# Optimization experiments

Measured on AMD Instinct MI355X. Metric: run time of the kernel, lower is better.

The kernel has to match this reference:

```python
import jax, jax.numpy as jnp
import numpy as np
import math

N = 131072   # number of points
C = 32       # embed_dim
K = 19       # num_class
ZD = 16      # z_dim
BN_EPS = 1e-4
SIG_THR = 0.8


def setup_inputs():
    key = jax.random.key(0)
    ks = jax.random.split(key, 16)
    f32 = jnp.float32
    rn = lambda k, s, sc=1.0: jax.random.normal(k, s, dtype=f32) * sc
    return {
        'feat': rn(ks[0], (N, C)),
        'scene_flow': rn(ks[1], (N, 3)),
        'coarse_pred': rn(ks[2], (N, K)),
        'z': rn(ks[3], (ZD,)),
        'select_w1': rn(ks[4], (C, C), 0.2),
        'bn_gamma': jnp.ones((C,), f32),
        'bn_beta': jnp.zeros((C,), f32),
        'bn_mean': jnp.zeros((C,), f32),
        'bn_var': jnp.ones((C,), f32),
        'select_w2': rn(ks[5], (C, 1), 0.2),
        'select_b2': jnp.zeros((1,), f32),
        'wq': rn(ks[6], (C, C), 0.2), 'bq': jnp.zeros((C,), f32),
        'wk': rn(ks[7], (C, C), 0.2), 'bk': jnp.zeros((C,), f32),
        'wv': rn(ks[8], (C, C), 0.2), 'bv': jnp.zeros((C,), f32),
        'wo': rn(ks[9], (C, C), 0.2), 'bo': jnp.zeros((C,), f32),
        'wt': rn(ks[10], (2 * C, C), 0.2), 'bt': jnp.zeros((C,), f32),
        'w_out': rn(ks[11], (C, K), 0.2), 'b_out': jnp.zeros((K,), f32),
        'w_gen': rn(ks[12], (ZD + K + 3, C), 0.2), 'b_gen': jnp.zeros((C,), f32),
    }


def _forward(feat, scene_flow, coarse_pred, z, select_w1, bn_gamma, bn_beta,
             bn_mean, bn_var, select_w2, select_b2, wq, bq, wk, bk, wv, bv,
             wo, bo, wt, bt, w_out, b_out, w_gen, b_gen):
    cp = jax.nn.softmax(coarse_pred, axis=-1)                      # (N, K)
    temp_mask = jnp.any(scene_flow != 0, axis=-1)                  # (N,)
    # select_mlp: Linear(no bias) -> BatchNorm(eval, eps=1e-4) -> ReLU -> Linear -> Sigmoid
    h = (feat @ select_w1 - bn_mean) / jnp.sqrt(bn_var + BN_EPS) * bn_gamma + bn_beta
    h = jnp.maximum(h, 0.0)
    score = jax.nn.sigmoid(h @ select_w2 + select_b2)[:, 0]        # (N,)
    valid = (score < SIG_THR) & temp_mask                          # (N,)
    # cvae stand-in: linear over concat(z, onehot(class), scene_flow) -> (N, K, C)
    wz, wc, ws = w_gen[:ZD], w_gen[ZD:ZD + K], w_gen[ZD + K:]
    gen = (z @ wz + b_gen)[None, None, :] + wc[None, :, :] + (scene_flow @ ws)[:, None, :]
    gen = gen * cp[:, :, None]                                     # scale by softmax prob
    # tiny cross-attention: 1 query per point over K=19 class prototypes
    q = feat @ wq + bq                                             # (N, C)
    k_ = jnp.einsum('nkc,cd->nkd', gen, wk) + bk                   # (N, K, C)
    v_ = jnp.einsum('nkc,cd->nkd', gen, wv) + bv                   # (N, K, C)
    attn = jax.nn.softmax(jnp.einsum('nd,nkd->nk', q, k_) / math.sqrt(C), axis=-1)
    aug = jnp.einsum('nk,nkd->nd', attn, v_) @ wo + bo             # (N, C)
    # scatter-back: invalid points get zeros (equivalent to torch boolean scatter)
    new_feat = jnp.where(valid[:, None], aug, 0.0)
    refine = jnp.concatenate([feat, new_feat], axis=-1) @ wt + bt  # (N, C)
    return refine @ w_out + b_out                                  # (N, K)


def reference(feat, scene_flow, coarse_pred, z, select_w1, bn_gamma, bn_beta,
              bn_mean, bn_var, select_w2, select_b2, wq, bq, wk, bk, wv, bv,
              wo, bo, wt, bt, w_out, b_out, w_gen, b_gen):
    return _forward(feat, scene_flow, coarse_pred, z, select_w1, bn_gamma,
                    bn_beta, bn_mean, bn_var, select_w2, select_b2, wq, bq,
                    wk, bk, wv, bv, wo, bo, wt, bt, w_out, b_out, w_gen, b_gen)
```

## Files before the change

kernel.cpp:

```cpp
#include <hip/hip_runtime.h>

#define NPTS 131072

constexpr int OFF_SW1 = 0;
constexpr int OFF_BNS = 1024;
constexpr int OFF_BNH = 1056;
constexpr int OFF_SW2 = 1088;
constexpr int OFF_B2  = 1120;
constexpr int TBL  = 1152;
constexpr int TQG  = 1152;
constexpr int TA1  = 1760;
constexpr int TGVB = 2368;
constexpr int TMVB = 2729;
constexpr int TQM  = 2786;
constexpr int TQBV = 2882;
constexpr int TQGB = 2914;
constexpr int TBB  = 2933;
constexpr int TCV  = 2952;
constexpr int TQMB = 2971;
constexpr int TQBB = 2974;
constexpr int LQG  = 0,    LA1  = 608,  LGVB = 1216, LMVB = 1577;
constexpr int LQM  = 1634, LQBV = 1730, LQGB = 1762, LBB  = 1781;
constexpr int LCV  = 1800, LQMB = 1819, LQBB = 1822;
constexpr int XG   = 3072;
constexpr int XA2  = 3680;
constexpr int XMK  = 4288;
constexpr int XMV  = 4384;
constexpr int XGK  = 4480;
constexpr int XGV  = 5088;
constexpr int XB   = 5696;

#define CONST_AS __attribute__((address_space(4)))
__device__ __forceinline__ const CONST_AS float* to_const(const float* p) {
    return (const CONST_AS float*)p;
}

__global__ __launch_bounds__(256) void pre_a(
    const float* __restrict__ z,
    const float* __restrict__ sw1,
    const float* __restrict__ bn_gamma, const float* __restrict__ bn_beta,
    const float* __restrict__ bn_mean,  const float* __restrict__ bn_var,
    const float* __restrict__ sw2,      const float* __restrict__ sb2,
    const float* __restrict__ wq, const float* __restrict__ bq,
    const float* __restrict__ wk, const float* __restrict__ bk,
    const float* __restrict__ wv,
    const float* __restrict__ wt, const float* __restrict__ bt,
    const float* __restrict__ wout, const float* __restrict__ bout,
    const float* __restrict__ wgen, const float* __restrict__ bgen,
    float* __restrict__ W)
{
    int i = blockIdx.x * 256 + threadIdx.x;
    if (i < 1024) {
        W[OFF_SW1 + i] = sw1[(i & 31) * 32 + (i >> 5)];
    } else if (i < 1632) {
        int t = i - 1024, e = t / 19, j = t % 19;
        float a1 = 0.f, a2 = 0.f;
        for (int d = 0; d < 32; ++d) {
            float w_ = wout[d*19 + j];
            a1 += wt[e*32 + d] * w_;
            a2 += wt[(32 + e)*32 + d] * w_;
        }
        W[TA1 + t] = a1; W[XA2 + t] = a2;
    } else if (i < 2240) {
        int t = i - 1632, k = t >> 5, e = t & 31;
        float g = bgen[e];
        for (int d = 0; d < 16; ++d) g += z[d] * wgen[d*32 + e];
        W[XG + t] = g + wgen[(16 + k)*32 + e];
    } else if (i < 2336) {
        int t = i - 2240, m = t >> 5, c = t & 31;
        float a = 0.f, b = 0.f;
        for (int e = 0; e < 32; ++e) {
            float wsr = wgen[(35 + m)*32 + e];
            a += wsr * wk[e*32 + c];
            b += wsr * wv[e*32 + c];
        }
        W[XMK + t] = a; W[XMV + t] = b;
    } else if (i < 2368) {
        int t = i - 2336;
        float scale = bn_gamma[t] / sqrtf(bn_var[t] + 1e-4f);
        W[OFF_BNS + t] = scale;
        W[OFF_BNH + t] = bn_beta[t] - bn_mean[t] * scale;
        W[OFF_SW2 + t] = sw2[t];
    } else if (i < 2387) {
        int t = i - 2368;
        float a = bout[t];
        for (int d = 0; d < 32; ++d) a += bt[d] * wout[d*19 + t];
        W[TBB + t] = a;
    } else if (i < 2419) {
        int t = i - 2387;
        float a = 0.f;
        for (int c = 0; c < 32; ++c) a += wq[t*32 + c] * bk[c];
        W[TQBV + t] = a;
    } else if (i == 2419) {
        W[OFF_B2] = sb2[0];
    } else if (i == 2420) {
        float a = 0.f;
        for (int c = 0; c < 32; ++c) a += bq[c] * bk[c];
        W[TQBB] = a;
    } else if (i == 2421) {
        W[TBL + 1823] = 0.f;
    }
}

__global__ __launch_bounds__(256) void pre_b(
    const float* __restrict__ wq, const float* __restrict__ bq,
    const float* __restrict__ wk, const float* __restrict__ wv,
    const float* __restrict__ wo,
    float* __restrict__ W)
{
    int i = blockIdx.x * 256 + threadIdx.x;
    if (i < 608) {
        int k = i >> 5, c = i & 31;
        float a = 0.f, b = 0.f;
        for (int e = 0; e < 32; ++e) {
            float g = W[XG + k*32 + e];
            a += g * wk[e*32 + c];
            b += g * wv[e*32 + c];
        }
        W[XGK + i] = a; W[XGV + i] = b;
    } else if (i < 1216) {
        int t = i - 608, c = t / 19, j = t % 19;
        float a = 0.f;
        for (int d = 0; d < 32; ++d) a += wo[c*32 + d] * W[XA2 + d*19 + j];
        W[XB + t] = a;
    } else if (i < 1312) {
        int t = i - 1216, e = t / 3, m = t % 3;
        float a = 0.f;
        for (int c = 0; c < 32; ++c) a += wq[e*32 + c] * W[XMK + m*32 + c];
        W[TQM + t] = a;
    } else if (i < 1315) {
        int m = i - 1312;
        float a = 0.f;
        for (int c = 0; c < 32; ++c) a += bq[c] * W[XMK + m*32 + c];
        W[TQMB + m] = a;
    }
}

__global__ __launch_bounds__(256) void pre_c(
    const float* __restrict__ wq, const float* __restrict__ bq,
    const float* __restrict__ bv, const float* __restrict__ bo,
    float* __restrict__ W)
{
    int i = blockIdx.x * 256 + threadIdx.x;
    if (i < 608) {
        int e = i / 19, k = i % 19;
        float a = 0.f;
        for (int c = 0; c < 32; ++c) a += wq[e*32 + c] * W[XGK + k*32 + c];
        W[TQG + i] = a;
    } else if (i < 627) {
        int k = i - 608;
        float a = 0.f;
        for (int c = 0; c < 32; ++c) a += bq[c] * W[XGK + k*32 + c];
        W[TQGB + k] = a;
    } else if (i < 988) {
        int t = i - 627, k = t / 19, j = t % 19;
        float a = 0.f;
        for (int c = 0; c < 32; ++c) a += W[XGV + k*32 + c] * W[XB + c*19 + j];
        W[TGVB + t] = a;
    } else if (i < 1045) {
        int t = i - 988, m = t / 19, j = t % 19;
        float a = 0.f;
        for (int c = 0; c < 32; ++c) a += W[XMV + m*32 + c] * W[XB + c*19 + j];
        W[TMVB + t] = a;
    } else if (i < 1064) {
        int j = i - 1045;
        float a = 0.f;
        for (int c = 0; c < 32; ++c) a += bv[c] * W[XB + c*19 + j];
        for (int d = 0; d < 32; ++d) a += bo[d] * W[XA2 + d*19 + j];
        W[TCV + j] = a;
    }
}

__global__ __launch_bounds__(256, 1) void main_k(
    const float* __restrict__ feat,
    const float* __restrict__ sflow,
    const float* __restrict__ cpred,
    const float* __restrict__ Wg,
    float* __restrict__ out)
{
    const CONST_AS float* W = to_const(Wg);
    const int n = blockIdx.x * 256 + threadIdx.x;
    const int t = threadIdx.x;

    __shared__ float T[1824];
    {
        const float4* src = (const float4*)(Wg + TBL);
        float4* dst = (float4*)T;
        dst[t] = src[t];
        if (t < 200) dst[256 + t] = src[256 + t];
    }
    __syncthreads();

    float f[32];
    const float4* fp = (const float4*)(feat + (long)n * 32);
#pragma unroll
    for (int g = 0; g < 8; ++g) {
        float4 v = fp[g];
        f[g*4+0] = v.x; f[g*4+1] = v.y; f[g*4+2] = v.z; f[g*4+3] = v.w;
    }
    float s0 = sflow[(long)n*3 + 0];
    float s1 = sflow[(long)n*3 + 1];
    float s2 = sflow[(long)n*3 + 2];
    bool tmask = (s0 != 0.f) | (s1 != 0.f) | (s2 != 0.f);

    float cp[19];
#pragma unroll
    for (int k = 0; k < 19; ++k) cp[k] = cpred[(long)n*19 + k];
    float m1 = cp[0];
#pragma unroll
    for (int k = 1; k < 19; ++k) m1 = fmaxf(m1, cp[k]);
    float sum1 = 0.f;
#pragma unroll
    for (int k = 0; k < 19; ++k) { cp[k] = __expf(cp[k] - m1); sum1 += cp[k]; }
    float r1 = 1.f / sum1;
#pragma unroll
    for (int k = 0; k < 19; ++k) cp[k] *= r1;

    float sacc = W[OFF_B2];
#pragma unroll
    for (int c = 0; c < 32; ++c) {
        float a = 0.f;
#pragma unroll
        for (int e = 0; e < 32; ++e) a = fmaf(f[e], W[OFF_SW1 + c*32 + e], a);
        float h = fmaf(a, W[OFF_BNS + c], W[OFF_BNH + c]);
        h = fmaxf(h, 0.f);
        sacc = fmaf(h, W[OFF_SW2 + c], sacc);
    }
    bool valid = tmask && (sacc < 1.3862943611198906f);

    float qg[19], o[19];
#pragma unroll
    for (int k = 0; k < 19; ++k) { qg[k] = T[LQGB + k]; o[k] = T[LBB + k]; }
    float qm0 = T[LQMB + 0], qm1 = T[LQMB + 1], qm2 = T[LQMB + 2];
    float qb = T[LQBB];
#pragma unroll 4
    for (int e = 0; e < 32; ++e) {
        float fe = f[e];
#pragma unroll
        for (int k = 0; k < 19; ++k) {
            qg[k] = fmaf(fe, T[LQG + e*19 + k], qg[k]);
            o[k]  = fmaf(fe, T[LA1 + e*19 + k], o[k]);
        }
        qm0 = fmaf(fe, T[LQM + e*3 + 0], qm0);
        qm1 = fmaf(fe, T[LQM + e*3 + 1], qm1);
        qm2 = fmaf(fe, T[LQM + e*3 + 2], qm2);
        qb  = fmaf(fe, T[LQBV + e], qb);
    }
    float qs = s0*qm0 + s1*qm1 + s2*qm2;

    const float RS = 0.17677669529663687f;
    float l[19];
#pragma unroll
    for (int k = 0; k < 19; ++k) l[k] = fmaf(cp[k], qg[k] + qs, qb) * RS;

    float m2 = l[0];
#pragma unroll
    for (int k = 1; k < 19; ++k) m2 = fmaxf(m2, l[k]);
    float sum2 = 0.f;
#pragma unroll
    for (int k = 0; k < 19; ++k) { l[k] = __expf(l[k] - m2); sum2 += l[k]; }
    float r2 = 1.f / sum2;
    float Sw = 0.f;
#pragma unroll
    for (int k = 0; k < 19; ++k) { l[k] = l[k] * r2 * cp[k]; Sw += l[k]; }

    float a2[19];
#pragma unroll
    for (int j = 0; j < 19; ++j) a2[j] = T[LCV + j];
    float cms[3] = { Sw * s0, Sw * s1, Sw * s2 };
#pragma unroll
    for (int m = 0; m < 3; ++m) {
        float cm = cms[m];
#pragma unroll
        for (int j = 0; j < 19; ++j) a2[j] = fmaf(cm, T[LMVB + m*19 + j], a2[j]);
    }
#pragma unroll 4
    for (int k = 0; k < 19; ++k) {
        float lk = l[k];
#pragma unroll
        for (int j = 0; j < 19; ++j) a2[j] = fmaf(lk, T[LGVB + k*19 + j], a2[j]);
    }

    float vg = valid ? 1.f : 0.f;
    float* op = out + (long)n * 19;
#pragma unroll
    for (int j = 0; j < 19; ++j) op[j] = fmaf(vg, a2[j], o[j]);
}

extern "C" void kernel_launch(void* const* d_in, const int* in_sizes, int n_in,
                              void* d_out, int out_size, void* d_ws, size_t ws_size,
                              hipStream_t stream) {
    const float* feat  = (const float*)d_in[0];
    const float* sflow = (const float*)d_in[1];
    const float* cpred = (const float*)d_in[2];
    const float* z     = (const float*)d_in[3];
    const float* sw1   = (const float*)d_in[4];
    const float* bn_g  = (const float*)d_in[5];
    const float* bn_b  = (const float*)d_in[6];
    const float* bn_m  = (const float*)d_in[7];
    const float* bn_v  = (const float*)d_in[8];
    const float* sw2   = (const float*)d_in[9];
    const float* sb2   = (const float*)d_in[10];
    const float* wq    = (const float*)d_in[11];
    const float* bq    = (const float*)d_in[12];
    const float* wk    = (const float*)d_in[13];
    const float* bk    = (const float*)d_in[14];
    const float* wv    = (const float*)d_in[15];
    const float* bv    = (const float*)d_in[16];
    const float* wo    = (const float*)d_in[17];
    const float* bo    = (const float*)d_in[18];
    const float* wt    = (const float*)d_in[19];
    const float* bt    = (const float*)d_in[20];
    const float* wout  = (const float*)d_in[21];
    const float* bout  = (const float*)d_in[22];
    const float* wgen  = (const float*)d_in[23];
    const float* bgen  = (const float*)d_in[24];

    float* W = (float*)d_ws;

    hipLaunchKernelGGL(pre_a, dim3(10), dim3(256), 0, stream,
                       z, sw1, bn_g, bn_b, bn_m, bn_v, sw2, sb2,
                       wq, bq, wk, bk, wv, wt, bt, wout, bout, wgen, bgen, W);
    hipLaunchKernelGGL(pre_b, dim3(6), dim3(256), 0, stream,
                       wq, bq, wk, wv, wo, W);
    hipLaunchKernelGGL(pre_c, dim3(5), dim3(256), 0, stream,
                       wq, bq, bv, bo, W);

    hipLaunchKernelGGL(main_k, dim3(NPTS / 256), dim3(256), 0, stream,
                       feat, sflow, cpred, W, (float*)d_out);
}
```

Before: 167.8 us.

## Process two points per thread and pad weight tables to 20-wide rows

The main kernel now has each thread handle two points, n and n+65536, and launches 256 blocks instead of 512. Each LDS and constant weight load then feeds FMAs for both points. The per-class weight tables are repacked with a row stride of 20, filling a 2048-float shared table. The per-point q·bk bias term is dropped because it is constant across classes and cancels in the softmax, which removes two precompute branches. The cost is roughly double the register pressure per thread and fewer waves per CU, which may hurt latency hiding.

```diff
diff --git a/kernel.cpp b/kernel.cpp
--- a/kernel.cpp
+++ b/kernel.cpp
@@ -1,6 +1,7 @@
 #include <hip/hip_runtime.h>
 
 #define NPTS 131072
+#define HALFN 65536
 
 constexpr int OFF_SW1 = 0;
 constexpr int OFF_BNS = 1024;
@@ -8,27 +9,22 @@
 constexpr int OFF_SW2 = 1088;
 constexpr int OFF_B2  = 1120;
 constexpr int TBL  = 1152;
-constexpr int TQG  = 1152;
-constexpr int TA1  = 1760;
-constexpr int TGVB = 2368;
-constexpr int TMVB = 2729;
-constexpr int TQM  = 2786;
-constexpr int TQBV = 2882;
-constexpr int TQGB = 2914;
-constexpr int TBB  = 2933;
-constexpr int TCV  = 2952;
-constexpr int TQMB = 2971;
-constexpr int TQBB = 2974;
-constexpr int LQG  = 0,    LA1  = 608,  LGVB = 1216, LMVB = 1577;
-constexpr int LQM  = 1634, LQBV = 1730, LQGB = 1762, LBB  = 1781;
-constexpr int LCV  = 1800, LQMB = 1819, LQBB = 1822;
-constexpr int XG   = 3072;
-constexpr int XA2  = 3680;
-constexpr int XMK  = 4288;
-constexpr int XMV  = 4384;
-constexpr int XGK  = 4480;
-constexpr int XGV  = 5088;
-constexpr int XB   = 5696;
+constexpr int LQG  = 0;
+constexpr int LA1  = 640;
+constexpr int LGVB = 1280;
+constexpr int LMVB = 1660;
+constexpr int LQM  = 1720;
+constexpr int LQGB = 1848;
+constexpr int LBB  = 1868;
+constexpr int LCV  = 1888;
+constexpr int LQMB = 1908;
+constexpr int XG   = 3328;
+constexpr int XA2  = 3936;
+constexpr int XMK  = 4544;
+constexpr int XMV  = 4640;
+constexpr int XGK  = 4736;
+constexpr int XGV  = 5344;
+constexpr int XB   = 5952;
 
 #define CONST_AS __attribute__((address_space(4)))
 __device__ __forceinline__ const CONST_AS float* to_const(const float* p) {
@@ -41,8 +37,7 @@
     const float* __restrict__ bn_gamma, const float* __restrict__ bn_beta,
     const float* __restrict__ bn_mean,  const float* __restrict__ bn_var,
     const float* __restrict__ sw2,      const float* __restrict__ sb2,
-    const float* __restrict__ wq, const float* __restrict__ bq,
-    const float* __restrict__ wk, const float* __restrict__ bk,
+    const float* __restrict__ wk,
     const float* __restrict__ wv,
     const float* __restrict__ wt, const float* __restrict__ bt,
     const float* __restrict__ wout, const float* __restrict__ bout,
@@ -60,7 +55,7 @@
             a1 += wt[e*32 + d] * w_;
             a2 += wt[(32 + e)*32 + d] * w_;
         }
-        W[TA1 + t] = a1; W[XA2 + t] = a2;
+        W[TBL + LA1 + e*20 + j] = a1; W[XA2 + t] = a2;
     } else if (i < 2240) {
         int t = i - 1632, k = t >> 5, e = t & 31;
         float g = bgen[e];
@@ -85,20 +80,9 @@
         int t = i - 2368;
         float a = bout[t];
         for (int d = 0; d < 32; ++d) a += bt[d] * wout[d*19 + t];
-        W[TBB + t] = a;
-    } else if (i < 2419) {
-        int t = i - 2387;
-        float a = 0.f;
-        for (int c = 0; c < 32; ++c) a += wq[t*32 + c] * bk[c];
-        W[TQBV + t] = a;
-    } else if (i == 2419) {
+        W[TBL + LBB + t] = a;
+    } else if (i == 2387) {
         W[OFF_B2] = sb2[0];
-    } else if (i == 2420) {
-        float a = 0.f;
-        for (int c = 0; c < 32; ++c) a += bq[c] * bk[c];
-        W[TQBB] = a;
-    } else if (i == 2421) {
-        W[TBL + 1823] = 0.f;
     }
 }
 
@@ -127,12 +111,12 @@
         int t = i - 1216, e = t / 3, m = t % 3;
         float a = 0.f;
         for (int c = 0; c < 32; ++c) a += wq[e*32 + c] * W[XMK + m*32 + c];
-        W[TQM + t] = a;
+        W[TBL + LQM + e*4 + m] = a;
     } else if (i < 1315) {
         int m = i - 1312;
         float a = 0.f;
         for (int c = 0; c < 32; ++c) a += bq[c] * W[XMK + m*32 + c];
-        W[TQMB + m] = a;
+        W[TBL + LQMB + m] = a;
     }
 }
 
@@ -146,28 +130,28 @@
         int e = i / 19, k = i % 19;
         float a = 0.f;
         for (int c = 0; c < 32; ++c) a += wq[e*32 + c] * W[XGK + k*32 + c];
-        W[TQG + i] = a;
+        W[TBL + LQG + e*20 + k] = a;
     } else if (i < 627) {
         int k = i - 608;
         float a = 0.f;
         for (int c = 0; c < 32; ++c) a += bq[c] * W[XGK + k*32 + c];
-        W[TQGB + k] = a;
+        W[TBL + LQGB + k] = a;
     } else if (i < 988) {
         int t = i - 627, k = t / 19, j = t % 19;
         float a = 0.f;
         for (int c = 0; c < 32; ++c) a += W[XGV + k*32 + c] * W[XB + c*19 + j];
-        W[TGVB + t] = a;
+        W[TBL + LGVB + k*20 + j] = a;
     } else if (i < 1045) {
         int t = i - 988, m = t / 19, j = t % 19;
         float a = 0.f;
         for (int c = 0; c < 32; ++c) a += W[XMV + m*32 + c] * W[XB + c*19 + j];
-        W[TMVB + t] = a;
+        W[TBL + LMVB + m*20 + j] = a;
     } else if (i < 1064) {
         int j = i - 1045;
         float a = 0.f;
         for (int c = 0; c < 32; ++c) a += bv[c] * W[XB + c*19 + j];
         for (int d = 0; d < 32; ++d) a += bo[d] * W[XA2 + d*19 + j];
-        W[TCV + j] = a;
+        W[TBL + LCV + j] = a;
     }
 }
 
@@ -179,112 +163,165 @@
     float* __restrict__ out)
 {
     const CONST_AS float* W = to_const(Wg);
-    const int n = blockIdx.x * 256 + threadIdx.x;
     const int t = threadIdx.x;
-
-    __shared__ float T[1824];
+    const int n0 = blockIdx.x * 256 + t;
+    const int n1 = n0 + HALFN;
+
+    __shared__ float T[2048];
     {
         const float4* src = (const float4*)(Wg + TBL);
         float4* dst = (float4*)T;
         dst[t] = src[t];
-        if (t < 200) dst[256 + t] = src[256 + t];
+        dst[256 + t] = src[256 + t];
     }
     __syncthreads();
 
-    float f[32];
-    const float4* fp = (const float4*)(feat + (long)n * 32);
-#pragma unroll
-    for (int g = 0; g < 8; ++g) {
-        float4 v = fp[g];
-        f[g*4+0] = v.x; f[g*4+1] = v.y; f[g*4+2] = v.z; f[g*4+3] = v.w;
-    }
-    float s0 = sflow[(long)n*3 + 0];
-    float s1 = sflow[(long)n*3 + 1];
-    float s2 = sflow[(long)n*3 + 2];
-    bool tmask = (s0 != 0.f) | (s1 != 0.f) | (s2 != 0.f);
-
-    float cp[19];
-#pragma unroll
-    for (int k = 0; k < 19; ++k) cp[k] = cpred[(long)n*19 + k];
-    float m1 = cp[0];
-#pragma unroll
-    for (int k = 1; k < 19; ++k) m1 = fmaxf(m1, cp[k]);
-    float sum1 = 0.f;
-#pragma unroll
-    for (int k = 0; k < 19; ++k) { cp[k] = __expf(cp[k] - m1); sum1 += cp[k]; }
-    float r1 = 1.f / sum1;
-#pragma unroll
-    for (int k = 0; k < 19; ++k) cp[k] *= r1;
-
-    float sacc = W[OFF_B2];
-#pragma unroll
+    float f0[32], f1[32];
+    {
+        const float4* p0 = (const float4*)(feat + (long)n0 * 32);
+        const float4* p1 = (const float4*)(feat + (long)n1 * 32);
+#pragma unroll
+        for (int g = 0; g < 8; ++g) {
+            float4 v = p0[g];
+            f0[g*4+0] = v.x; f0[g*4+1] = v.y; f0[g*4+2] = v.z; f0[g*4+3] = v.w;
+            float4 u = p1[g];
+            f1[g*4+0] = u.x; f1[g*4+1] = u.y; f1[g*4+2] = u.z; f1[g*4+3] = u.w;
+        }
+    }
+    float s00 = sflow[(long)n0*3+0], s01 = sflow[(long)n0*3+1], s02 = sflow[(long)n0*3+2];
+    float s10 = sflow[(long)n1*3+0], s11 = sflow[(long)n1*3+1], s12 = sflow[(long)n1*3+2];
+    bool tm0 = (s00 != 0.f) | (s01 != 0.f) | (s02 != 0.f);
+    bool tm1 = (s10 != 0.f) | (s11 != 0.f) | (s12 != 0.f);
+
+    float cp0[19], cp1[19];
+#pragma unroll
+    for (int k = 0; k < 19; ++k) {
+        cp0[k] = cpred[(long)n0*19 + k];
+        cp1[k] = cpred[(long)n1*19 + k];
+    }
+    float m0 = cp0[0], m1_ = cp1[0];
+#pragma unroll
+    for (int k = 1; k < 19; ++k) { m0 = fmaxf(m0, cp0[k]); m1_ = fmaxf(m1_, cp1[k]); }
+    float su0 = 0.f, su1 = 0.f;
+#pragma unroll
+    for (int k = 0; k < 19; ++k) {
+        cp0[k] = __expf(cp0[k] - m0);  su0 += cp0[k];
+        cp1[k] = __expf(cp1[k] - m1_); su1 += cp1[k];
+    }
+    float ri0 = 1.f / su0, ri1 = 1.f / su1;
+#pragma unroll
+    for (int k = 0; k < 19; ++k) { cp0[k] *= ri0; cp1[k] *= ri1; }
+
+    float sa0 = W[OFF_B2], sa1 = W[OFF_B2];
+#pragma unroll 4
     for (int c = 0; c < 32; ++c) {
-        float a = 0.f;
-#pragma unroll
-        for (int e = 0; e < 32; ++e) a = fmaf(f[e], W[OFF_SW1 + c*32 + e], a);
-        float h = fmaf(a, W[OFF_BNS + c], W[OFF_BNH + c]);
-        h = fmaxf(h, 0.f);
-        sacc = fmaf(h, W[OFF_SW2 + c], sacc);
-    }
-    bool valid = tmask && (sacc < 1.3862943611198906f);
-
-    float qg[19], o[19];
-#pragma unroll
-    for (int k = 0; k < 19; ++k) { qg[k] = T[LQGB + k]; o[k] = T[LBB + k]; }
-    float qm0 = T[LQMB + 0], qm1 = T[LQMB + 1], qm2 = T[LQMB + 2];
-    float qb = T[LQBB];
+        float a0 = 0.f, a1 = 0.f;
+#pragma unroll
+        for (int e = 0; e < 32; ++e) {
+            float w_ = W[OFF_SW1 + c*32 + e];
+            a0 = fmaf(f0[e], w_, a0);
+            a1 = fmaf(f1[e], w_, a1);
+        }
+        float bs = W[OFF_BNS + c], bh = W[OFF_BNH + c], w2 = W[OFF_SW2 + c];
+        float h0 = fmaxf(fmaf(a0, bs, bh), 0.f);
+        float h1 = fmaxf(fmaf(a1, bs, bh), 0.f);
+        sa0 = fmaf(h0, w2, sa0);
+        sa1 = fmaf(h1, w2, sa1);
+    }
+    bool valid0 = tm0 && (sa0 < 1.3862943611198906f);
+    bool valid1 = tm1 && (sa1 < 1.3862943611198906f);
+
+    float qg0[19], qg1[19], o0[19], o1[19];
+#pragma unroll
+    for (int k = 0; k < 19; ++k) {
+        float g = T[LQGB + k], b = T[LBB + k];
+        qg0[k] = g; qg1[k] = g; o0[k] = b; o1[k] = b;
+    }
+    float qmA0 = T[LQMB+0], qmA1 = T[LQMB+1], qmA2 = T[LQMB+2];
+    float qmB0 = qmA0, qmB1 = qmA1, qmB2 = qmA2;
 #pragma unroll 4
     for (int e = 0; e < 32; ++e) {
-        float fe = f[e];
+        float fe0 = f0[e], fe1 = f1[e];
 #pragma unroll
         for (int k = 0; k < 19; ++k) {
-            qg[k] = fmaf(fe, T[LQG + e*19 + k], qg[k]);
-            o[k]  = fmaf(fe, T[LA1 + e*19 + k], o[k]);
-        }
-        qm0 = fmaf(fe, T[LQM + e*3 + 0], qm0);
-        qm1 = fmaf(fe, T[LQM + e*3 + 1], qm1);
-        qm2 = fmaf(fe, T[LQM + e*3 + 2], qm2);
-        qb  = fmaf(fe, T[LQBV + e], qb);
-    }
-    float qs = s0*qm0 + s1*qm1 + s2*qm2;
+            float w_ = T[LQG + e*20 + k];
+            qg0[k] = fmaf(fe0, w_, qg0[k]);
+            qg1[k] = fmaf(fe1, w_, qg1[k]);
+        }
+#pragma unroll
+        for (int k = 0; k < 19; ++k) {
+            float w_ = T[LA1 + e*20 + k];
+            o0[k] = fmaf(fe0, w_, o0[k]);
+            o1[k] = fmaf(fe1, w_, o1[k]);
+        }
+        float q0 = T[LQM + e*4 + 0], q1 = T[LQM + e*4 + 1], q2 = T[LQM + e*4 + 2];
+        qmA0 = fmaf(fe0, q0, qmA0); qmA1 = fmaf(fe0, q1, qmA1); qmA2 = fmaf(fe0, q2, qmA2);
+        qmB0 = fmaf(fe1, q0, qmB0); qmB1 = fmaf(fe1, q1, qmB1); qmB2 = fmaf(fe1, q2, qmB2);
+    }
+    float qs0 = s00*qmA0 + s01*qmA1 + s02*qmA2;
+    float qs1 = s10*qmB0 + s11*qmB1 + s12*qmB2;
 
     const float RS = 0.17677669529663687f;
-    float l[19];
-#pragma unroll
-    for (int k = 0; k < 19; ++k) l[k] = fmaf(cp[k], qg[k] + qs, qb) * RS;
-
-    float m2 = l[0];
-#pragma unroll
-    for (int k = 1; k < 19; ++k) m2 = fmaxf(m2, l[k]);
-    float sum2 = 0.f;
-#pragma unroll
-    for (int k = 0; k < 19; ++k) { l[k] = __expf(l[k] - m2); sum2 += l[k]; }
-    float r2 = 1.f / sum2;
-    float Sw = 0.f;
-#pragma unroll
-    for (int k = 0; k < 19; ++k) { l[k] = l[k] * r2 * cp[k]; Sw += l[k]; }
-
-    float a2[19];
-#pragma unroll
-    for (int j = 0; j < 19; ++j) a2[j] = T[LCV + j];
-    float cms[3] = { Sw * s0, Sw * s1, Sw * s2 };
+    float l0[19], l1[19];
+#pragma unroll
+    for (int k = 0; k < 19; ++k) {
+        l0[k] = (cp0[k] * (qg0[k] + qs0)) * RS;
+        l1[k] = (cp1[k] * (qg1[k] + qs1)) * RS;
+    }
+
+    float x0 = l0[0], x1 = l1[0];
+#pragma unroll
+    for (int k = 1; k < 19; ++k) { x0 = fmaxf(x0, l0[k]); x1 = fmaxf(x1, l1[k]); }
+    float t0 = 0.f, t1 = 0.f;
+#pragma unroll
+    for (int k = 0; k < 19; ++k) {
+        l0[k] = __expf(l0[k] - x0); t0 += l0[k];
+        l1[k] = __expf(l1[k] - x1); t1 += l1[k];
+    }
+    float r20 = 1.f / t0, r21 = 1.f / t1;
+    float Sw0 = 0.f, Sw1 = 0.f;
+#pragma unroll
+    for (int k = 0; k < 19; ++k) {
+        l0[k] = l0[k] * r20 * cp0[k]; Sw0 += l0[k];
+        l1[k] = l1[k] * r21 * cp1[k]; Sw1 += l1[k];
+    }
+
+    float a20[19], a21[19];
+#pragma unroll
+    for (int j = 0; j < 19; ++j) { float c = T[LCV + j]; a20[j] = c; a21[j] = c; }
+    float cA0 = Sw0*s00, cA1 = Sw0*s01, cA2 = Sw0*s02;
+    float cB0 = Sw1*s10, cB1 = Sw1*s11, cB2 = Sw1*s12;
 #pragma unroll
     for (int m = 0; m < 3; ++m) {
-        float cm = cms[m];
-#pragma unroll
-        for (int j = 0; j < 19; ++j) a2[j] = fmaf(cm, T[LMVB + m*19 + j], a2[j]);
+        float ca = (m == 0) ? cA0 : (m == 1 ? cA1 : cA2);
+        float cb = (m == 0) ? cB0 : (m == 1 ? cB1 : cB2);
+#pragma unroll
+        for (int j = 0; j < 19; ++j) {
+            float w_ = T[LMVB + m*20 + j];
+            a20[j] = fmaf(ca, w_, a20[j]);
+            a21[j] = fmaf(cb, w_, a21[j]);
+        }
     }
 #pragma unroll 4
     for (int k = 0; k < 19; ++k) {
-        float lk = l[k];
-#pragma unroll
-        for (int j = 0; j < 19; ++j) a2[j] = fmaf(lk, T[LGVB + k*19 + j], a2[j]);
-    }
-
-    float vg = valid ? 1.f : 0.f;
-    float* op = out + (long)n * 19;
-#pragma unroll
-    for (int j = 0; j < 19; ++j) op[j] = fmaf(vg, a2[j], o[j]);
+        float lk0 = l0[k], lk1 = l1[k];
+#pragma unroll
+        for (int j = 0; j < 19; ++j) {
+            float w_ = T[LGVB + k*20 + j];
+            a20[j] = fmaf(lk0, w_, a20[j]);
+            a21[j] = fmaf(lk1, w_, a21[j]);
+        }
+    }
+
+    float vg0 = valid0 ? 1.f : 0.f;
+    float vg1 = valid1 ? 1.f : 0.f;
+    float* op0 = out + (long)n0 * 19;
+    float* op1 = out + (long)n1 * 19;
+#pragma unroll
+    for (int j = 0; j < 19; ++j) {
+        op0[j] = fmaf(vg0, a20[j], o0[j]);
+        op1[j] = fmaf(vg1, a21[j], o1[j]);
+    }
 }
 
 extern "C" void kernel_launch(void* const* d_in, const int* in_sizes, int n_in,
@@ -304,7 +341,7 @@
     const float* wq    = (const float*)d_in[11];
     const float* bq    = (const float*)d_in[12];
     const float* wk    = (const float*)d_in[13];
-    const float* bk    = (const float*)d_in[14];
+    const float* bk    = (const float*)d_in[14];  (void)bk;
     const float* wv    = (const float*)d_in[15];
     const float* bv    = (const float*)d_in[16];
     const float* wo    = (const float*)d_in[17];
@@ -320,12 +357,12 @@
 
     hipLaunchKernelGGL(pre_a, dim3(10), dim3(256), 0, stream,
                        z, sw1, bn_g, bn_b, bn_m, bn_v, sw2, sb2,
-                       wq, bq, wk, bk, wv, wt, bt, wout, bout, wgen, bgen, W);
+                       wk, wv, wt, bt, wout, bout, wgen, bgen, W);
     hipLaunchKernelGGL(pre_b, dim3(6), dim3(256), 0, stream,
                        wq, bq, wk, wv, wo, W);
     hipLaunchKernelGGL(pre_c, dim3(5), dim3(256), 0, stream,
                        wq, bq, bv, bo, W);
 
-    hipLaunchKernelGGL(main_k, dim3(NPTS / 256), dim3(256), 0, stream,
+    hipLaunchKernelGGL(main_k, dim3(256), dim3(256), 0, stream,
                        feat, sflow, cpred, W, (float*)d_out);
 }
```

Result: faster. 157.9 us (-5.9%).

## Pad LDS tables, stage feat in shared memory, drop softmax-invariant bias terms

Applied to the files above, without the earlier changes.

Reorganizes the precomputed shared-memory tables into padded, interleaved rows of stride 40 and 20, aligned for vector LDS reads. It also stages each thread's feature vector into a transposed shared buffer so the second projection loop reads from LDS instead of holding 32 registers live, and raises launch bounds to 2 blocks per CU. The per-point bias term qb is removed from the attention logits, because a constant added to every logit does not change the softmax, and its precompute is dropped. The goal is lower register pressure and higher occupancy, at the cost of 32 KB of extra LDS per block and extra LDS traffic.

```diff
diff --git a/kernel.cpp b/kernel.cpp
--- a/kernel.cpp
+++ b/kernel.cpp
@@ -8,27 +8,21 @@
 constexpr int OFF_SW2 = 1088;
 constexpr int OFF_B2  = 1120;
 constexpr int TBL  = 1152;
-constexpr int TQG  = 1152;
-constexpr int TA1  = 1760;
-constexpr int TGVB = 2368;
-constexpr int TMVB = 2729;
-constexpr int TQM  = 2786;
-constexpr int TQBV = 2882;
-constexpr int TQGB = 2914;
-constexpr int TBB  = 2933;
-constexpr int TCV  = 2952;
-constexpr int TQMB = 2971;
-constexpr int TQBB = 2974;
-constexpr int LQG  = 0,    LA1  = 608,  LGVB = 1216, LMVB = 1577;
-constexpr int LQM  = 1634, LQBV = 1730, LQGB = 1762, LBB  = 1781;
-constexpr int LCV  = 1800, LQMB = 1819, LQBB = 1822;
-constexpr int XG   = 3072;
-constexpr int XA2  = 3680;
-constexpr int XMK  = 4288;
-constexpr int XMV  = 4384;
-constexpr int XGK  = 4480;
-constexpr int XGV  = 5088;
-constexpr int XB   = 5696;
+constexpr int LQA  = 0;
+constexpr int LGVB = 1280;
+constexpr int LMVB = 1660;
+constexpr int LQM  = 1720;
+constexpr int LQGB = 1848;
+constexpr int LBB  = 1868;
+constexpr int LCV  = 1888;
+constexpr int LQMB = 1908;
+constexpr int XG   = 3328;
+constexpr int XA2  = 3936;
+constexpr int XMK  = 4544;
+constexpr int XMV  = 4640;
+constexpr int XGK  = 4736;
+constexpr int XGV  = 5344;
+constexpr int XB   = 5952;
 
 #define CONST_AS __attribute__((address_space(4)))
 __device__ __forceinline__ const CONST_AS float* to_const(const float* p) {
@@ -41,8 +35,7 @@
     const float* __restrict__ bn_gamma, const float* __restrict__ bn_beta,
     const float* __restrict__ bn_mean,  const float* __restrict__ bn_var,
     const float* __restrict__ sw2,      const float* __restrict__ sb2,
-    const float* __restrict__ wq, const float* __restrict__ bq,
-    const float* __restrict__ wk, const float* __restrict__ bk,
+    const float* __restrict__ wk,
     const float* __restrict__ wv,
     const float* __restrict__ wt, const float* __restrict__ bt,
     const float* __restrict__ wout, const float* __restrict__ bout,
@@ -60,7 +53,7 @@
             a1 += wt[e*32 + d] * w_;
             a2 += wt[(32 + e)*32 + d] * w_;
         }
-        W[TA1 + t] = a1; W[XA2 + t] = a2;
+        W[TBL + LQA + e*40 + 20 + j] = a1; W[XA2 + t] = a2;
     } else if (i < 2240) {
         int t = i - 1632, k = t >> 5, e = t & 31;
         float g = bgen[e];
@@ -85,20 +78,13 @@
         int t = i - 2368;
         float a = bout[t];
         for (int d = 0; d < 32; ++d) a += bt[d] * wout[d*19 + t];
-        W[TBB + t] = a;
-    } else if (i < 2419) {
-        int t = i - 2387;
-        float a = 0.f;
-        for (int c = 0; c < 32; ++c) a += wq[t*32 + c] * bk[c];
-        W[TQBV + t] = a;
-    } else if (i == 2419) {
+        W[TBL + LBB + t] = a;
+    } else if (i == 2387) {
         W[OFF_B2] = sb2[0];
-    } else if (i == 2420) {
-        float a = 0.f;
-        for (int c = 0; c < 32; ++c) a += bq[c] * bk[c];
-        W[TQBB] = a;
-    } else if (i == 2421) {
-        W[TBL + 1823] = 0.f;
+    } else if (i < 2452) {
+        int t = i - 2388;
+        if (t < 32)      W[TBL + LQA + t*40 + 19] = 0.f;
+        else             W[TBL + LQA + (t-32)*40 + 39] = 0.f;
     }
 }
 
@@ -127,12 +113,17 @@
         int t = i - 1216, e = t / 3, m = t % 3;
         float a = 0.f;
         for (int c = 0; c < 32; ++c) a += wq[e*32 + c] * W[XMK + m*32 + c];
-        W[TQM + t] = a;
+        W[TBL + LQM + e*4 + m] = a;
     } else if (i < 1315) {
         int m = i - 1312;
         float a = 0.f;
         for (int c = 0; c < 32; ++c) a += bq[c] * W[XMK + m*32 + c];
-        W[TQMB + m] = a;
+        W[TBL + LQMB + m] = a;
+    } else if (i < 1347) {
+        int e = i - 1315;
+        W[TBL + LQM + e*4 + 3] = 0.f;
+    } else if (i == 1347) {
+        W[TBL + LQMB + 3] = 0.f;
     }
 }
 
@@ -146,32 +137,39 @@
         int e = i / 19, k = i % 19;
         float a = 0.f;
         for (int c = 0; c < 32; ++c) a += wq[e*32 + c] * W[XGK + k*32 + c];
-        W[TQG + i] = a;
+        W[TBL + LQA + e*40 + k] = a;
     } else if (i < 627) {
         int k = i - 608;
         float a = 0.f;
         for (int c = 0; c < 32; ++c) a += bq[c] * W[XGK + k*32 + c];
-        W[TQGB + k] = a;
+        W[TBL + LQGB + k] = a;
     } else if (i < 988) {
         int t = i - 627, k = t / 19, j = t % 19;
         float a = 0.f;
         for (int c = 0; c < 32; ++c) a += W[XGV + k*32 + c] * W[XB + c*19 + j];
-        W[TGVB + t] = a;
+        W[TBL + LGVB + k*20 + j] = a;
     } else if (i < 1045) {
         int t = i - 988, m = t / 19, j = t % 19;
         float a = 0.f;
         for (int c = 0; c < 32; ++c) a += W[XMV + m*32 + c] * W[XB + c*19 + j];
-        W[TMVB + t] = a;
+        W[TBL + LMVB + m*20 + j] = a;
     } else if (i < 1064) {
         int j = i - 1045;
         float a = 0.f;
         for (int c = 0; c < 32; ++c) a += bv[c] * W[XB + c*19 + j];
         for (int d = 0; d < 32; ++d) a += bo[d] * W[XA2 + d*19 + j];
-        W[TCV + j] = a;
-    }
-}
-
-__global__ __launch_bounds__(256, 1) void main_k(
+        W[TBL + LCV + j] = a;
+    } else if (i < 1108) {
+        int t = i - 1064;
+        if (t < 19)      W[TBL + LGVB + t*20 + 19] = 0.f;
+        else if (t < 22) W[TBL + LMVB + (t-19)*20 + 19] = 0.f;
+        else if (t == 22) W[TBL + LQGB + 19] = 0.f;
+        else if (t == 23) W[TBL + LBB + 19] = 0.f;
+        else if (t == 24) W[TBL + LCV + 19] = 0.f;
+    }
+}
+
+__global__ __launch_bounds__(256, 2) void main_k(
     const float* __restrict__ feat,
     const float* __restrict__ sflow,
     const float* __restrict__ cpred,
@@ -179,25 +177,32 @@
     float* __restrict__ out)
 {
     const CONST_AS float* W = to_const(Wg);
-    const int n = blockIdx.x * 256 + threadIdx.x;
     const int t = threadIdx.x;
-
-    __shared__ float T[1824];
+    const int n = blockIdx.x * 256 + t;
+
+    __shared__ __align__(16) float T[1912];
+    __shared__ float F[32 * 256];
+
     {
         const float4* src = (const float4*)(Wg + TBL);
         float4* dst = (float4*)T;
         dst[t] = src[t];
-        if (t < 200) dst[256 + t] = src[256 + t];
-    }
+        if (t < 222) dst[256 + t] = src[256 + t];
+    }
+
+    float f[32];
+    {
+        const float4* fp = (const float4*)(feat + (long)n * 32);
+#pragma unroll
+        for (int g = 0; g < 8; ++g) {
+            float4 v = fp[g];
+            f[g*4+0] = v.x; f[g*4+1] = v.y; f[g*4+2] = v.z; f[g*4+3] = v.w;
+        }
+    }
+#pragma unroll
+    for (int e = 0; e < 32; ++e) F[e*256 + t] = f[e];
     __syncthreads();
 
-    float f[32];
-    const float4* fp = (const float4*)(feat + (long)n * 32);
-#pragma unroll
-    for (int g = 0; g < 8; ++g) {
-        float4 v = fp[g];
-        f[g*4+0] = v.x; f[g*4+1] = v.y; f[g*4+2] = v.z; f[g*4+3] = v.w;
-    }
     float s0 = sflow[(long)n*3 + 0];
     float s1 = sflow[(long)n*3 + 1];
     float s2 = sflow[(long)n*3 + 2];
@@ -217,13 +222,12 @@
     for (int k = 0; k < 19; ++k) cp[k] *= r1;
 
     float sacc = W[OFF_B2];
-#pragma unroll
+#pragma unroll 2
     for (int c = 0; c < 32; ++c) {
         float a = 0.f;
 #pragma unroll
         for (int e = 0; e < 32; ++e) a = fmaf(f[e], W[OFF_SW1 + c*32 + e], a);
-        float h = fmaf(a, W[OFF_BNS + c], W[OFF_BNH + c]);
-        h = fmaxf(h, 0.f);
+        float h = fmaxf(fmaf(a, W[OFF_BNS + c], W[OFF_BNH + c]), 0.f);
         sacc = fmaf(h, W[OFF_SW2 + c], sacc);
     }
     bool valid = tmask && (sacc < 1.3862943611198906f);
@@ -232,26 +236,23 @@
 #pragma unroll
     for (int k = 0; k < 19; ++k) { qg[k] = T[LQGB + k]; o[k] = T[LBB + k]; }
     float qm0 = T[LQMB + 0], qm1 = T[LQMB + 1], qm2 = T[LQMB + 2];
-    float qb = T[LQBB];
 #pragma unroll 4
     for (int e = 0; e < 32; ++e) {
-        float fe = f[e];
-#pragma unroll
-        for (int k = 0; k < 19; ++k) {
-            qg[k] = fmaf(fe, T[LQG + e*19 + k], qg[k]);
-            o[k]  = fmaf(fe, T[LA1 + e*19 + k], o[k]);
-        }
-        qm0 = fmaf(fe, T[LQM + e*3 + 0], qm0);
-        qm1 = fmaf(fe, T[LQM + e*3 + 1], qm1);
-        qm2 = fmaf(fe, T[LQM + e*3 + 2], qm2);
-        qb  = fmaf(fe, T[LQBV + e], qb);
+        float fe = F[e*256 + t];
+#pragma unroll
+        for (int k = 0; k < 19; ++k) qg[k] = fmaf(fe, T[LQA + e*40 + k], qg[k]);
+#pragma unroll
+        for (int k = 0; k < 19; ++k) o[k]  = fmaf(fe, T[LQA + e*40 + 20 + k], o[k]);
+        qm0 = fmaf(fe, T[LQM + e*4 + 0], qm0);
+        qm1 = fmaf(fe, T[LQM + e*4 + 1], qm1);
+        qm2 = fmaf(fe, T[LQM + e*4 + 2], qm2);
     }
     float qs = s0*qm0 + s1*qm1 + s2*qm2;
 
     const float RS = 0.17677669529663687f;
     float l[19];
 #pragma unroll
-    for (int k = 0; k < 19; ++k) l[k] = fmaf(cp[k], qg[k] + qs, qb) * RS;
+    for (int k = 0; k < 19; ++k) l[k] = (cp[k] * (qg[k] + qs)) * RS;
 
     float m2 = l[0];
 #pragma unroll
@@ -267,18 +268,18 @@
     float a2[19];
 #pragma unroll
     for (int j = 0; j < 19; ++j) a2[j] = T[LCV + j];
-    float cms[3] = { Sw * s0, Sw * s1, Sw * s2 };
-#pragma unroll
-    for (int m = 0; m < 3; ++m) {
-        float cm = cms[m];
-#pragma unroll
-        for (int j = 0; j < 19; ++j) a2[j] = fmaf(cm, T[LMVB + m*19 + j], a2[j]);
-    }
-#pragma unroll 4
+    float c0 = Sw * s0, c1 = Sw * s1, c2 = Sw * s2;
+#pragma unroll
+    for (int j = 0; j < 19; ++j) a2[j] = fmaf(c0, T[LMVB + j], a2[j]);
+#pragma unroll
+    for (int j = 0; j < 19; ++j) a2[j] = fmaf(c1, T[LMVB + 20 + j], a2[j]);
+#pragma unroll
+    for (int j = 0; j < 19; ++j) a2[j] = fmaf(c2, T[LMVB + 40 + j], a2[j]);
+#pragma unroll
     for (int k = 0; k < 19; ++k) {
         float lk = l[k];
 #pragma unroll
-        for (int j = 0; j < 19; ++j) a2[j] = fmaf(lk, T[LGVB + k*19 + j], a2[j]);
+        for (int j = 0; j < 19; ++j) a2[j] = fmaf(lk, T[LGVB + k*20 + j], a2[j]);
     }
 
     float vg = valid ? 1.f : 0.f;
@@ -304,7 +305,7 @@
     const float* wq    = (const float*)d_in[11];
     const float* bq    = (const float*)d_in[12];
     const float* wk    = (const float*)d_in[13];
-    const float* bk    = (const float*)d_in[14];
+    const float* bk    = (const float*)d_in[14];  (void)bk;
     const float* wv    = (const float*)d_in[15];
     const float* bv    = (const float*)d_in[16];
     const float* wo    = (const float*)d_in[17];
@@ -320,12 +321,12 @@
 
     hipLaunchKernelGGL(pre_a, dim3(10), dim3(256), 0, stream,
                        z, sw1, bn_g, bn_b, bn_m, bn_v, sw2, sb2,
-                       wq, bq, wk, bk, wv, wt, bt, wout, bout, wgen, bgen, W);
+                       wk, wv, wt, bt, wout, bout, wgen, bgen, W);
     hipLaunchKernelGGL(pre_b, dim3(6), dim3(256), 0, stream,
                        wq, bq, wk, wv, wo, W);
     hipLaunchKernelGGL(pre_c, dim3(5), dim3(256), 0, stream,
                        wq, bq, bv, bo, W);
 
-    hipLaunchKernelGGL(main_k, dim3(NPTS / 256), dim3(256), 0, stream,
+    hipLaunchKernelGGL(main_k, dim3(512), dim3(256), 0, stream,
                        feat, sflow, cpred, W, (float*)d_out);
 }
```

Measured after the change: 150.9 us. -10.1%, faster.
